# Optimization experiments

Hardware: AMD Instinct MI355X
Metric: run time of the kernel (lower is better)

The kernel has to match this reference:

```python
import jax, jax.numpy as jnp
import numpy as np

NX, NY, NZ = 432, 496, 1
VX, VY, VZ = 0.16, 0.16, 4.0
XOFF = VX / 2 + 0.0
YOFF = VY / 2 + (-39.68)
ZOFF = VZ / 2 + (-3.0)
GRID = NZ * NX * NY
P, NPT, B = 100000, 32, 8
EPS = 1e-3


def setup_inputs() -> dict:
    key = jax.random.key(0)
    k1, k2, k3, k4 = jax.random.split(key, 4)
    voxels = jax.random.normal(k1, (P, NPT, 4), dtype=jnp.float32)
    num_points = jax.random.randint(k2, (P,), 1, NPT + 1, dtype=jnp.int32)
    b = jax.random.randint(k3, (P,), 0, B, dtype=jnp.int32)
    # unique BEV cells (17 coprime with GRID, P < GRID) -> deterministic scatter
    cell = (jnp.arange(P, dtype=jnp.int32) * 17) % GRID
    y = cell // NX
    x = cell % NX
    coords = jnp.stack([b, jnp.zeros_like(b), y, x], axis=1)  # [P,4] (b,z,y,x)
    W = jax.random.normal(k4, (64, 10), dtype=jnp.float32) * 0.1
    gamma = jnp.ones((64,), dtype=jnp.float32)
    beta = jnp.zeros((64,), dtype=jnp.float32)
    return {"voxels": voxels, "num_points": num_points, "coords": coords,
            "W": W, "gamma": gamma, "beta": beta}


def reference(voxels, num_points, coords, W, gamma, beta):
    cf = coords.astype(voxels.dtype)
    npf = num_points.astype(voxels.dtype)
    # cluster feature: offset from pillar mean
    points_mean = voxels[:, :, :3].sum(axis=1, keepdims=True) / npf[:, None, None]
    f_cluster = voxels[:, :, :3] - points_mean
    # center feature: offset from voxel center
    cx = cf[:, 3, None] * VX + XOFF
    cy = cf[:, 2, None] * VY + YOFF
    cz = cf[:, 1, None] * VZ + ZOFF
    f_center = jnp.stack([voxels[:, :, 0] - cx,
                          voxels[:, :, 1] - cy,
                          voxels[:, :, 2] - cz], axis=-1)
    feat = jnp.concatenate([voxels, f_cluster, f_center], axis=-1)  # [P,N,10]
    mask = (jnp.arange(NPT, dtype=jnp.int32)[None, :] < num_points[:, None])
    feat = feat * mask.astype(feat.dtype)[:, :, None]
    # linear(10->64, no bias) + BatchNorm1d (batch stats, biased var) + relu
    x = jnp.einsum('pnf,cf->pnc', feat, W)  # [P,N,64]
    mean = x.mean(axis=(0, 1))
    var = ((x - mean) ** 2).mean(axis=(0, 1))
    x = (x - mean) * jax.lax.rsqrt(var + EPS) * gamma + beta
    x = jax.nn.relu(x)
    pillars = x.max(axis=1)  # [P,64]
    idx = coords[:, 1] + coords[:, 2] * NX + coords[:, 3]
    bev = jnp.zeros((B, GRID, 64), dtype=pillars.dtype)
    bev = bev.at[coords[:, 0], idx].set(pillars)
    bev = jnp.transpose(bev, (0, 2, 1))  # [B,64,GRID]
    return bev.reshape(B, 64 * NZ, NY, NX)
```

## Files before the change

### kernel.cpp

```cpp
#include <hip/hip_runtime.h>

typedef unsigned short u16;

#define NXg 432
#define NYg 496
#define GRIDg (NXg*NYg)
#define NPTg 32
#define Bg 8
#define CHg 64
#define NSLOT 32

__device__ __forceinline__ float bf2f(u16 u){
    union { unsigned int i; float f; } x; x.i = ((unsigned int)u) << 16; return x.f;
}
__device__ __forceinline__ u16 f2bf(float f){
    union { float f; unsigned int i; } x; x.f = f;
    unsigned int i = x.i + 0x7FFFu + ((x.i >> 16) & 1u);
    return (u16)(i >> 16);
}
__device__ __forceinline__ bool is_bf16(const void* gamma){
    return ((*(const unsigned*)gamma) & 0xFFFFu) != 0u;
}

__global__ __launch_bounds__(256) void k_init(int* __restrict__ map, float* __restrict__ chsum){
    int t = blockIdx.x*256 + threadIdx.x;
    ((int4*)map)[t] = make_int4(-1,-1,-1,-1);
    if (t < (NSLOT*128)/4) ((float4*)chsum)[t] = make_float4(0.f,0.f,0.f,0.f);
}

__global__ __launch_bounds__(256) void k_pillar(
    const void* __restrict__ vox, const int* __restrict__ nump,
    const int* __restrict__ coords, const void* __restrict__ Wv,
    const void* __restrict__ gv,
    u16* __restrict__ pmax, u16* __restrict__ pmin,
    int* __restrict__ map, float* __restrict__ chsum,
    int P, int nwaves)
{
    const bool isbf = is_bf16(gv);
    __shared__ float4 stage[4][NPTg];
    int lane = threadIdx.x & 63;
    int wv   = threadIdx.x >> 6;
    int wid  = (blockIdx.x*256 + threadIdx.x) >> 6;
    int n    = lane & 31;

    float w4,w5,w6,w7,w8,w9, wp0,wp1,wp2,wp3;
    {
        float w[10];
#pragma unroll
        for (int j=0;j<10;j++)
            w[j] = isbf ? bf2f(((const u16*)Wv)[lane*10 + j]) : ((const float*)Wv)[lane*10 + j];
        wp0 = w[0]+w[4]+w[7];
        wp1 = w[1]+w[5]+w[8];
        wp2 = w[2]+w[6]+w[9];
        wp3 = w[3];
        w4=w[4]; w5=w[5]; w6=w[6]; w7=w[7]; w8=w[8]; w9=w[9];
    }

    float sx = 0.f, sx2 = 0.f;

    for (int p = wid; p < P; p += nwaves) {
        int np = nump[p];
        int4 cc = *(const int4*)(coords + 4*p);

        if (lane < 32) {
            float4 pt;
            if (isbf){
                ushort4 raw = *(const ushort4*)((const u16*)vox + ((size_t)p*NPTg + n)*4);
                pt = make_float4(bf2f(raw.x), bf2f(raw.y), bf2f(raw.z), bf2f(raw.w));
            } else {
                pt = *(const float4*)((const float*)vox + ((size_t)p*NPTg + n)*4);
            }
            stage[wv][n] = pt;
        }

        float qmx = -3e38f, qmn = 3e38f, sq = 0.f, sq2 = 0.f;
        float sa0 = 0.f, sa1 = 0.f, sa2 = 0.f;
#pragma unroll
        for (int k = 0; k < NPTg; k++){
            float4 a = stage[wv][k];
            sa0 += a.x; sa1 += a.y; sa2 += a.z;
            float q = fmaf(a.x, wp0, fmaf(a.y, wp1, fmaf(a.z, wp2, a.w*wp3)));
            if (k < np){
                qmx = fmaxf(qmx, q);
                qmn = fminf(qmn, q);
                sq += q;
                sq2 = fmaf(q, q, sq2);
            }
        }
        float inv = 1.0f / (float)np;
        float m0 = sa0*inv, m1 = sa1*inv, m2 = sa2*inv;
        float ccx = (float)cc.w * 0.16f + 0.08f;
        float ccy = (float)cc.z * 0.16f + (0.08f - 39.68f);
        float ccz = (float)cc.y * 4.0f  + (2.0f - 3.0f);
        float d = -(m0*w4 + m1*w5 + m2*w6 + ccx*w7 + ccy*w8 + ccz*w9);

        float npf = (float)np;
        sx  += sq + npf*d;
        sx2 += sq2 + d*(2.f*sq + npf*d);

        float fmx = qmx + d, fmn = qmn + d;
        if (np < NPTg){ fmx = fmaxf(fmx, 0.f); fmn = fminf(fmn, 0.f); }
        pmax[(size_t)p*CHg + lane] = f2bf(fmx);
        pmin[(size_t)p*CHg + lane] = f2bf(fmn);
        if (lane == 0) map[cc.x*GRIDg + cc.z*NXg + cc.w] = p;
    }

    float* slot = chsum + (blockIdx.x & (NSLOT-1))*128;
    atomicAdd(slot + lane, sx);
    atomicAdd(slot + 64 + lane, sx2);
}

__global__ __launch_bounds__(64) void k_stats(
    const float* __restrict__ chsum,
    const void* __restrict__ gv, const void* __restrict__ bv,
    float* __restrict__ sb, int P)
{
    const bool isbf = is_bf16(gv);
    int t = threadIdx.x;
    float S = 0.f, S2 = 0.f;
    for (int sl = 0; sl < NSLOT; sl++){
        S  += chsum[sl*128 + t];
        S2 += chsum[sl*128 + 64 + t];
    }
    float cnt = (float)P * (float)NPTg;
    float mean = S / cnt;
    float var  = S2 / cnt - mean*mean;
    float g  = isbf ? bf2f(((const u16*)gv)[t]) : ((const float*)gv)[t];
    float be = isbf ? bf2f(((const u16*)bv)[t]) : ((const float*)bv)[t];
    float sc = g * rsqrtf(var + 1e-3f);
    float bi = be - mean*sc;
    sb[t] = sc; sb[64 + t] = bi;
}

__global__ __launch_bounds__(256) void k_gather(
    const int* __restrict__ map, const u16* __restrict__ pmax,
    const u16* __restrict__ pmin, const float* __restrict__ sb,
    const void* __restrict__ gv, void* __restrict__ out)
{
    const bool isbf = is_bf16(gv);
    const int G8 = GRIDg/8;
    int t  = blockIdx.x*256 + threadIdx.x;
    int g8 = t % G8;
    int q  = t / G8;
    int c0 = (q & 15) * 4;
    int b  = q >> 4;
    float sc[4], bi[4];
#pragma unroll
    for (int j = 0; j < 4; j++){ sc[j] = sb[c0+j]; bi[j] = sb[64+c0+j]; }

    const int* mp = map + (size_t)b*GRIDg + (size_t)g8*8;
    int4 mA = *(const int4*)mp;
    int4 mB = *(const int4*)(mp + 4);
    int pv[8] = {mA.x, mA.y, mA.z, mA.w, mB.x, mB.y, mB.z, mB.w};

    float r[4][8];
#pragma unroll
    for (int j = 0; j < 4; j++)
#pragma unroll
        for (int i = 0; i < 8; i++) r[j][i] = 0.f;

#pragma unroll
    for (int i = 0; i < 8; i++){
        int p = pv[i];
        if (p >= 0){
            uint2 ux = *(const uint2*)(pmax + (size_t)p*CHg + c0);
            uint2 un = *(const uint2*)(pmin + (size_t)p*CHg + c0);
            u16 hx[4] = {(u16)(ux.x & 0xFFFFu), (u16)(ux.x >> 16), (u16)(ux.y & 0xFFFFu), (u16)(ux.y >> 16)};
            u16 hn[4] = {(u16)(un.x & 0xFFFFu), (u16)(un.x >> 16), (u16)(un.y & 0xFFFFu), (u16)(un.y >> 16)};
#pragma unroll
            for (int j = 0; j < 4; j++){
                float v = bf2f((sc[j] >= 0.f) ? hx[j] : hn[j]);
                r[j][i] = fmaxf(fmaf(sc[j], v, bi[j]), 0.f);
            }
        }
    }

    size_t base = ((size_t)(b*CHg + c0))*GRIDg + (size_t)g8*8;
    if (isbf){
#pragma unroll
        for (int j = 0; j < 4; j++){
            union { u16 h[8]; uint4 v; } pk;
#pragma unroll
            for (int i = 0; i < 8; i++) pk.h[i] = f2bf(r[j][i]);
            *(uint4*)((u16*)out + base + (size_t)j*GRIDg) = pk.v;
        }
    } else {
#pragma unroll
        for (int j = 0; j < 4; j++){
            float4 a, bq;
            a.x = r[j][0]; a.y = r[j][1]; a.z = r[j][2]; a.w = r[j][3];
            bq.x = r[j][4]; bq.y = r[j][5]; bq.z = r[j][6]; bq.w = r[j][7];
            *(float4*)((float*)out + base + (size_t)j*GRIDg)     = a;
            *(float4*)((float*)out + base + (size_t)j*GRIDg + 4) = bq;
        }
    }
}

extern "C" void kernel_launch(void* const* d_in, const int* in_sizes, int n_in,
                              void* d_out, int out_size, void* d_ws, size_t ws_size,
                              hipStream_t stream)
{
    const void* vox   = d_in[0];
    const int* nump   = (const int*)d_in[1];
    const int* coords = (const int*)d_in[2];
    const void* Wv    = d_in[3];
    const void* gv    = d_in[4];
    const void* bv    = d_in[5];
    int P = in_sizes[1];

    float* chsum = (float*)d_ws;
    float* sb    = (float*)((char*)d_ws + 16384);
    u16*   pmax  = (u16*)((char*)d_ws + 32768);
    u16*   pmin  = pmax + (size_t)P*CHg;
    int*   map   = (int*)(pmin + (size_t)P*CHg);

    int initThreads = (Bg*GRIDg)/4;
    k_init<<<initThreads/256, 256, 0, stream>>>(map, chsum);

    int blocks1 = 2048;
    k_pillar<<<blocks1, 256, 0, stream>>>(vox, nump, coords, Wv, gv, pmax, pmin, map, chsum, P, blocks1*4);

    k_stats<<<1, 64, 0, stream>>>(chsum, gv, bv, sb, P);

    int total = Bg*16*(GRIDg/8);
    k_gather<<<total/256, 256, 0, stream>>>(map, pmax, pmin, sb, gv, d_out);
}
```

Baseline: 602.2 us.

## Use wave shuffles in pillar kernel and restructure gather to per-channel loop

The pillar kernel drops its LDS staging. It computes the point-mean sums with xor-shuffles across the wave, then walks only the valid points through readlane broadcasts instead of a masked fixed 32-iteration loop. The stats kernel now also writes a per-channel byte offset that picks the pmax or pmin buffer by the sign of the scale, so gather needs only one base pointer. Gather is remapped so each thread handles two BEV cells across all 64 channels, loading map entries once and writing two-element output stores per channel. This trades wide vector stores for narrow ones and uses scattered 2-byte reads per channel, which may hurt coalescing of the output writes.

Result: faster. 555.7 us (-7.7%).

```diff
diff --git a/kernel.cpp b/kernel.cpp
--- a/kernel.cpp
+++ b/kernel.cpp
@@ -21,14 +21,17 @@
 __device__ __forceinline__ bool is_bf16(const void* gamma){
     return ((*(const unsigned*)gamma) & 0xFFFFu) != 0u;
 }
-
-__global__ __launch_bounds__(256) void k_init(int* __restrict__ map, float* __restrict__ chsum){
+__device__ __forceinline__ float rdlane(float v, int k){
+    return __int_as_float(__builtin_amdgcn_readlane(__float_as_int(v), k));
+}
+
+__global__ __launch_bounds__(256) void pfe_init(int* __restrict__ map, float* __restrict__ chsum){
     int t = blockIdx.x*256 + threadIdx.x;
     ((int4*)map)[t] = make_int4(-1,-1,-1,-1);
     if (t < (NSLOT*128)/4) ((float4*)chsum)[t] = make_float4(0.f,0.f,0.f,0.f);
 }
 
-__global__ __launch_bounds__(256) void k_pillar(
+__global__ __launch_bounds__(256) void pfe_pillar(
     const void* __restrict__ vox, const int* __restrict__ nump,
     const int* __restrict__ coords, const void* __restrict__ Wv,
     const void* __restrict__ gv,
@@ -37,9 +40,7 @@
     int P, int nwaves)
 {
     const bool isbf = is_bf16(gv);
-    __shared__ float4 stage[4][NPTg];
     int lane = threadIdx.x & 63;
-    int wv   = threadIdx.x >> 6;
     int wid  = (blockIdx.x*256 + threadIdx.x) >> 6;
     int n    = lane & 31;
 
@@ -61,38 +62,40 @@
     for (int p = wid; p < P; p += nwaves) {
         int np = nump[p];
         int4 cc = *(const int4*)(coords + 4*p);
-
-        if (lane < 32) {
-            float4 pt;
-            if (isbf){
-                ushort4 raw = *(const ushort4*)((const u16*)vox + ((size_t)p*NPTg + n)*4);
-                pt = make_float4(bf2f(raw.x), bf2f(raw.y), bf2f(raw.z), bf2f(raw.w));
-            } else {
-                pt = *(const float4*)((const float*)vox + ((size_t)p*NPTg + n)*4);
-            }
-            stage[wv][n] = pt;
-        }
-
-        float qmx = -3e38f, qmn = 3e38f, sq = 0.f, sq2 = 0.f;
-        float sa0 = 0.f, sa1 = 0.f, sa2 = 0.f;
+        float4 pt;
+        if (isbf){
+            ushort4 raw = *(const ushort4*)((const u16*)vox + ((size_t)p*NPTg + n)*4);
+            pt = make_float4(bf2f(raw.x), bf2f(raw.y), bf2f(raw.z), bf2f(raw.w));
+        } else {
+            pt = *(const float4*)((const float*)vox + ((size_t)p*NPTg + n)*4);
+        }
+
+        float s0 = pt.x, s1 = pt.y, s2 = pt.z;
 #pragma unroll
-        for (int k = 0; k < NPTg; k++){
-            float4 a = stage[wv][k];
-            sa0 += a.x; sa1 += a.y; sa2 += a.z;
-            float q = fmaf(a.x, wp0, fmaf(a.y, wp1, fmaf(a.z, wp2, a.w*wp3)));
-            if (k < np){
-                qmx = fmaxf(qmx, q);
-                qmn = fminf(qmn, q);
-                sq += q;
-                sq2 = fmaf(q, q, sq2);
-            }
-        }
-        float inv = 1.0f / (float)np;
-        float m0 = sa0*inv, m1 = sa1*inv, m2 = sa2*inv;
+        for (int m = 1; m < 64; m <<= 1){
+            s0 += __shfl_xor(s0, m, 64);
+            s1 += __shfl_xor(s1, m, 64);
+            s2 += __shfl_xor(s2, m, 64);
+        }
+        float inv = 0.5f / (float)np;
+        float m0 = s0*inv, m1 = s1*inv, m2 = s2*inv;
         float ccx = (float)cc.w * 0.16f + 0.08f;
         float ccy = (float)cc.z * 0.16f + (0.08f - 39.68f);
         float ccz = (float)cc.y * 4.0f  + (2.0f - 3.0f);
         float d = -(m0*w4 + m1*w5 + m2*w6 + ccx*w7 + ccy*w8 + ccz*w9);
+
+        float qmx = -3e38f, qmn = 3e38f, sq = 0.f, sq2 = 0.f;
+        for (int k = 0; k < np; k++){
+            float ax = rdlane(pt.x, k);
+            float ay = rdlane(pt.y, k);
+            float az = rdlane(pt.z, k);
+            float aw = rdlane(pt.w, k);
+            float q = fmaf(ax, wp0, fmaf(ay, wp1, fmaf(az, wp2, aw*wp3)));
+            qmx = fmaxf(qmx, q);
+            qmn = fminf(qmn, q);
+            sq += q;
+            sq2 = fmaf(q, q, sq2);
+        }
 
         float npf = (float)np;
         sx  += sq + npf*d;
@@ -110,7 +113,7 @@
     atomicAdd(slot + 64 + lane, sx2);
 }
 
-__global__ __launch_bounds__(64) void k_stats(
+__global__ __launch_bounds__(64) void pfe_stats(
     const float* __restrict__ chsum,
     const void* __restrict__ gv, const void* __restrict__ bv,
     float* __restrict__ sb, int P)
@@ -130,68 +133,38 @@
     float sc = g * rsqrtf(var + 1e-3f);
     float bi = be - mean*sc;
     sb[t] = sc; sb[64 + t] = bi;
-}
-
-__global__ __launch_bounds__(256) void k_gather(
+    ((int*)sb)[128 + t] = (sc >= 0.f) ? 0 : P*CHg*2;
+}
+
+__global__ __launch_bounds__(192) void pfe_gather(
     const int* __restrict__ map, const u16* __restrict__ pmax,
-    const u16* __restrict__ pmin, const float* __restrict__ sb,
-    const void* __restrict__ gv, void* __restrict__ out)
+    const float* __restrict__ sb, const void* __restrict__ gv,
+    void* __restrict__ out)
 {
     const bool isbf = is_bf16(gv);
-    const int G8 = GRIDg/8;
-    int t  = blockIdx.x*256 + threadIdx.x;
-    int g8 = t % G8;
-    int q  = t / G8;
-    int c0 = (q & 15) * 4;
-    int b  = q >> 4;
-    float sc[4], bi[4];
+    int b  = blockIdx.y;
+    int px = blockIdx.x*384 + threadIdx.x*2;
+    int2 m2 = *(const int2*)(map + (size_t)b*GRIDg + px);
+    bool v0 = m2.x >= 0, v1 = m2.y >= 0;
+    int o0 = v0 ? m2.x*(CHg*2) : 0;
+    int o1 = v1 ? m2.y*(CHg*2) : 0;
+    const char* pb = (const char*)pmax;
+
 #pragma unroll
-    for (int j = 0; j < 4; j++){ sc[j] = sb[c0+j]; bi[j] = sb[64+c0+j]; }
-
-    const int* mp = map + (size_t)b*GRIDg + (size_t)g8*8;
-    int4 mA = *(const int4*)mp;
-    int4 mB = *(const int4*)(mp + 4);
-    int pv[8] = {mA.x, mA.y, mA.z, mA.w, mB.x, mB.y, mB.z, mB.w};
-
-    float r[4][8];
-#pragma unroll
-    for (int j = 0; j < 4; j++)
-#pragma unroll
-        for (int i = 0; i < 8; i++) r[j][i] = 0.f;
-
-#pragma unroll
-    for (int i = 0; i < 8; i++){
-        int p = pv[i];
-        if (p >= 0){
-            uint2 ux = *(const uint2*)(pmax + (size_t)p*CHg + c0);
-            uint2 un = *(const uint2*)(pmin + (size_t)p*CHg + c0);
-            u16 hx[4] = {(u16)(ux.x & 0xFFFFu), (u16)(ux.x >> 16), (u16)(ux.y & 0xFFFFu), (u16)(ux.y >> 16)};
-            u16 hn[4] = {(u16)(un.x & 0xFFFFu), (u16)(un.x >> 16), (u16)(un.y & 0xFFFFu), (u16)(un.y >> 16)};
-#pragma unroll
-            for (int j = 0; j < 4; j++){
-                float v = bf2f((sc[j] >= 0.f) ? hx[j] : hn[j]);
-                r[j][i] = fmaxf(fmaf(sc[j], v, bi[j]), 0.f);
-            }
-        }
-    }
-
-    size_t base = ((size_t)(b*CHg + c0))*GRIDg + (size_t)g8*8;
-    if (isbf){
-#pragma unroll
-        for (int j = 0; j < 4; j++){
-            union { u16 h[8]; uint4 v; } pk;
-#pragma unroll
-            for (int i = 0; i < 8; i++) pk.h[i] = f2bf(r[j][i]);
-            *(uint4*)((u16*)out + base + (size_t)j*GRIDg) = pk.v;
-        }
-    } else {
-#pragma unroll
-        for (int j = 0; j < 4; j++){
-            float4 a, bq;
-            a.x = r[j][0]; a.y = r[j][1]; a.z = r[j][2]; a.w = r[j][3];
-            bq.x = r[j][4]; bq.y = r[j][5]; bq.z = r[j][6]; bq.w = r[j][7];
-            *(float4*)((float*)out + base + (size_t)j*GRIDg)     = a;
-            *(float4*)((float*)out + base + (size_t)j*GRIDg + 4) = bq;
+    for (int c = 0; c < CHg; c++){
+        float sc = sb[c], bi = sb[64 + c];
+        int off = __builtin_amdgcn_readfirstlane(((const int*)sb)[128 + c]);
+        const char* base = pb + off;
+        float x0 = bf2f(*(const u16*)(base + o0 + c*2));
+        float x1 = bf2f(*(const u16*)(base + o1 + c*2));
+        float r0 = v0 ? fmaxf(fmaf(sc, x0, bi), 0.f) : 0.f;
+        float r1 = v1 ? fmaxf(fmaf(sc, x1, bi), 0.f) : 0.f;
+        size_t obase = ((size_t)(b*CHg + c))*GRIDg + px;
+        if (isbf){
+            unsigned pk = (unsigned)f2bf(r0) | ((unsigned)f2bf(r1) << 16);
+            *(unsigned*)((u16*)out + obase) = pk;
+        } else {
+            *(float2*)((float*)out + obase) = make_float2(r0, r1);
         }
     }
 }
@@ -215,13 +188,13 @@
     int*   map   = (int*)(pmin + (size_t)P*CHg);
 
     int initThreads = (Bg*GRIDg)/4;
-    k_init<<<initThreads/256, 256, 0, stream>>>(map, chsum);
+    pfe_init<<<initThreads/256, 256, 0, stream>>>(map, chsum);
 
     int blocks1 = 2048;
-    k_pillar<<<blocks1, 256, 0, stream>>>(vox, nump, coords, Wv, gv, pmax, pmin, map, chsum, P, blocks1*4);
-
-    k_stats<<<1, 64, 0, stream>>>(chsum, gv, bv, sb, P);
-
-    int total = Bg*16*(GRIDg/8);
-    k_gather<<<total/256, 256, 0, stream>>>(map, pmax, pmin, sb, gv, d_out);
-}
+    pfe_pillar<<<blocks1, 256, 0, stream>>>(vox, nump, coords, Wv, gv, pmax, pmin, map, chsum, P, blocks1*4);
+
+    pfe_stats<<<1, 64, 0, stream>>>(chsum, gv, bv, sb, P);
+
+    dim3 g3(GRIDg/384, Bg);
+    pfe_gather<<<g3, 192, 0, stream>>>(map, pmax, sb, gv, d_out);
+}
```
